# Performance work log

Hardware: AMD Instinct MI355X
Metric: run time of the kernel (lower is better)

Reference implementation:

```python
import jax, jax.numpy as jnp
import numpy as np

H, C = 4, 64          # heads, head_dim; H*C == hidden_channels == 256
HID = H * C
NT, NC = 50000, 10000
E_TT, E_CT = 400000, 200000
FT, FC = 128, 64


def _gat(xs, xd, att_s, att_d, bias, src, dst, num_dst):
    """PyG GATConv message passing. xs/xd: projected feats [Ns,H,C]/[Nd,H,C]."""
    a = (xs * att_s).sum(-1)[src] + (xd * att_d).sum(-1)[dst]      # [E,H]
    a = jax.nn.leaky_relu(a, 0.2)
    m = jax.ops.segment_max(a, dst, num_segments=num_dst)          # [Nd,H]
    m = jnp.where(jnp.isfinite(m), m, 0.0)
    ex = jnp.exp(a - m[dst])                                       # [E,H]
    den = jax.ops.segment_sum(ex, dst, num_segments=num_dst)       # [Nd,H]
    msg = jax.ops.segment_sum(ex[:, :, None] * xs[src], dst, num_segments=num_dst)  # [Nd,H,C]
    out = msg / jnp.maximum(den, 1e-16)[:, :, None]
    return out.reshape(num_dst, HID) + bias


def setup_inputs() -> dict:
    key = jax.random.key(0)
    ks = jax.random.split(key, 24)

    def glorot(k, shape):
        fan_in = shape[0] if len(shape) > 1 else shape[-1]
        return jax.random.normal(k, shape, jnp.float32) / np.sqrt(fan_in)

    inp = {
        'x_target': jax.random.normal(ks[0], (NT, FT), jnp.float32),
        'x_context': jax.random.normal(ks[1], (NC, FC), jnp.float32),
        'ei_tt': jax.random.randint(ks[2], (2, E_TT), 0, NT, jnp.int32),
        'ei_ct_src': jax.random.randint(ks[3], (E_CT,), 0, NC, jnp.int32),
        'ei_ct_dst': jax.random.randint(ks[4], (E_CT,), 0, NT, jnp.int32),
        # HeteroDictLinear pretransform
        'Wt': glorot(ks[5], (FT, HID)), 'bt': jnp.zeros((HID,), jnp.float32),
        'Wc': glorot(ks[6], (FC, HID)), 'bc': jnp.zeros((HID,), jnp.float32),
        # DirGATConv: src->dst GATConv
        'W_s2d': glorot(ks[7], (HID, HID)),
        'as_s2d': glorot(ks[8], (H, C)), 'ad_s2d': glorot(ks[9], (H, C)),
        'b_s2d': jnp.zeros((HID,), jnp.float32),
        # DirGATConv: dst->src GATConv
        'W_d2s': glorot(ks[10], (HID, HID)),
        'as_d2s': glorot(ks[11], (H, C)), 'ad_d2s': glorot(ks[12], (H, C)),
        'b_d2s': jnp.zeros((HID,), jnp.float32),
        # bipartite context->target GATConv
        'W_ct_src': glorot(ks[13], (HID, HID)), 'W_ct_dst': glorot(ks[14], (HID, HID)),
        'as_ct': glorot(ks[15], (H, C)), 'ad_ct': glorot(ks[16], (H, C)),
        'b_ct': jnp.zeros((HID,), jnp.float32),
        # final Linear(hidden, hidden)
        'W_out': glorot(ks[17], (HID, HID)), 'b_out': jnp.zeros((HID,), jnp.float32),
    }
    return inp


def reference(x_target, x_context, ei_tt, ei_ct_src, ei_ct_dst,
              Wt, bt, Wc, bc,
              W_s2d, as_s2d, ad_s2d, b_s2d,
              W_d2s, as_d2s, ad_d2s, b_d2s,
              W_ct_src, W_ct_dst, as_ct, ad_ct, b_ct,
              W_out, b_out):
    nt = x_target.shape[0]
    # HeteroDictLinear pretransform + relu
    ht = jax.nn.relu(x_target @ Wt + bt)      # [NT, HID]
    hc = jax.nn.relu(x_context @ Wc + bc)     # [NC, HID]

    # homogeneous target-target edges with self-loops (PyG GATConv default)
    loops = jnp.arange(nt, dtype=ei_tt.dtype)
    src = jnp.concatenate([ei_tt[0], loops])
    dst = jnp.concatenate([ei_tt[1], loops])

    # DirGATConv: (1-alpha)*conv(x, ei) + alpha*conv(x, ei^T), alpha=0.5
    p1 = (ht @ W_s2d).reshape(nt, H, C)
    out_s2d = _gat(p1, p1, as_s2d, ad_s2d, b_s2d, src, dst, nt)
    p2 = (ht @ W_d2s).reshape(nt, H, C)
    out_d2s = _gat(p2, p2, as_d2s, ad_d2s, b_d2s, dst, src, nt)
    out_tt = 0.5 * out_s2d + 0.5 * out_d2s

    # bipartite context->target GATConv (no self-loops)
    ps = (hc @ W_ct_src).reshape(hc.shape[0], H, C)
    pd = (ht @ W_ct_dst).reshape(nt, H, C)
    out_ct = _gat(ps, pd, as_ct, ad_ct, b_ct, ei_ct_src, ei_ct_dst, nt)

    # HeteroConv aggr='mean', then skip connection + relu, then final Linear
    x = (out_tt + out_ct) * 0.5
    x = jax.nn.relu(x + ht)
    return x @ W_out + b_out
```

## Files before the change

kernel.cpp:

```cpp
#include <hip/hip_runtime.h>
#include <hip/hip_bf16.h>
#include <cstdint>
#include <cstddef>


#define LRELU_SLOPE 0.2f
#define CAP 64
#define NRANGE 8

typedef __attribute__((ext_vector_type(8))) short short8;
typedef __attribute__((ext_vector_type(4))) float floatx4;

__device__ __forceinline__ float bf2f(ushort u) {
    union { unsigned int u32; float f; } v; v.u32 = ((unsigned int)u) << 16; return v.f;
}
__device__ __forceinline__ ushort f2bf(float x) {
    union { float f; unsigned int u; } v; v.f = x;
    unsigned int r = (v.u + 0x7FFFu + ((v.u >> 16) & 1u)) >> 16;
    return (ushort)r;
}

__global__ __launch_bounds__(256) void cast_bf16(
    const float* __restrict__ x, ushort* __restrict__ y, int n4)
{
    const int idx = blockIdx.x * blockDim.x + threadIdx.x;
    if (idx >= n4) return;
    float4 v = ((const float4*)x)[idx];
    ushort4 o;
    o.x = f2bf(v.x); o.y = f2bf(v.y); o.z = f2bf(v.z); o.w = f2bf(v.w);
    ((ushort4*)y)[idx] = o;
}

__global__ __launch_bounds__(256) void wtrans(
    const float* __restrict__ W, ushort* __restrict__ WT, int K)
{
    const int idx = blockIdx.x * blockDim.x + threadIdx.x;
    if (idx >= K * 256) return;
    const int k = idx >> 8, n = idx & 255;
    WT[n * K + k] = f2bf(W[idx]);
}

__global__ __launch_bounds__(256) void gemm_bf16(
    const ushort* __restrict__ A, const ushort* __restrict__ Bt,
    const float* __restrict__ bias, float* __restrict__ Cf,
    ushort* __restrict__ Cb, int M, int K, int do_relu,
    const float* __restrict__ attS, const float* __restrict__ attD,
    float* __restrict__ aSo, float* __restrict__ aDo)
{
    __shared__ short As[64][40];
    __shared__ short Bs[64][40];
    const int tid  = threadIdx.x;
    const int row0 = blockIdx.x * 64;
    const int col0 = blockIdx.y * 64;
    const int lr = tid >> 2;
    const int lk = (tid & 3) * 8;
    const int w    = tid >> 6;
    const int lane = tid & 63;
    const int mrow = 16 * w + (lane & 15);
    const int ksel = (lane >> 4) * 8;

    floatx4 acc0 = {0.f,0.f,0.f,0.f}, acc1 = acc0, acc2 = acc0, acc3 = acc0;

    for (int k0 = 0; k0 < K; k0 += 32) {
        short8 av = {0,0,0,0,0,0,0,0};
        if (row0 + lr < M)
            av = *(const short8*)(A + (size_t)(row0 + lr) * K + k0 + lk);
        *(short8*)&As[lr][lk] = av;
        *(short8*)&Bs[lr][lk] =
            *(const short8*)(Bt + (size_t)(col0 + lr) * K + k0 + lk);
        __syncthreads();
        short8 af = *(const short8*)&As[mrow][ksel];
        short8 b0 = *(const short8*)&Bs[ 0 + (lane & 15)][ksel];
        short8 b1 = *(const short8*)&Bs[16 + (lane & 15)][ksel];
        short8 b2 = *(const short8*)&Bs[32 + (lane & 15)][ksel];
        short8 b3 = *(const short8*)&Bs[48 + (lane & 15)][ksel];
        acc0 = __builtin_amdgcn_mfma_f32_16x16x32_bf16(af, b0, acc0, 0, 0, 0);
        acc1 = __builtin_amdgcn_mfma_f32_16x16x32_bf16(af, b1, acc1, 0, 0, 0);
        acc2 = __builtin_amdgcn_mfma_f32_16x16x32_bf16(af, b2, acc2, 0, 0, 0);
        acc3 = __builtin_amdgcn_mfma_f32_16x16x32_bf16(af, b3, acc3, 0, 0, 0);
        __syncthreads();
    }

    const int rbase = row0 + 16 * w + (lane >> 4) * 4;
    floatx4 av[4] = {acc0, acc1, acc2, acc3};
#pragma unroll
    for (int c = 0; c < 4; ++c) {
        const int col = col0 + 16 * c + (lane & 15);
        const float bv = bias ? bias[col] : 0.f;
#pragma unroll
        for (int i = 0; i < 4; ++i) {
            const int row = rbase + i;
            if (row < M) {
                float v = av[c][i] + bv;
                if (do_relu) v = fmaxf(v, 0.f);
                const size_t off = (size_t)row * 256 + col;
                if (Cf) Cf[off] = v;
                if (Cb) Cb[off] = f2bf(v);
            }
        }
    }

    if (attS) {
        const int cix = lane & 15;
        float sA[4] = {0.f,0.f,0.f,0.f}, sD[4] = {0.f,0.f,0.f,0.f};
#pragma unroll
        for (int c = 0; c < 4; ++c) {
            const float as_v = attS[col0 + 16 * c + cix];
            const float ad_v = attD ? attD[col0 + 16 * c + cix] : 0.f;
#pragma unroll
            for (int i = 0; i < 4; ++i) {
                sA[i] += av[c][i] * as_v;
                sD[i] += av[c][i] * ad_v;
            }
        }
#pragma unroll
        for (int off = 1; off < 16; off <<= 1) {
#pragma unroll
            for (int i = 0; i < 4; ++i) {
                sA[i] += __shfl_xor(sA[i], off);
                sD[i] += __shfl_xor(sD[i], off);
            }
        }
        if (cix == 0) {
            const int head = col0 >> 6;
#pragma unroll
            for (int i = 0; i < 4; ++i) {
                const int row = rbase + i;
                if (row < M) {
                    aSo[(size_t)row * 4 + head] = sA[i];
                    if (aDo) aDo[(size_t)row * 4 + head] = sD[i];
                }
            }
        }
    }
}

__global__ void fold_ct(const float* __restrict__ W, const float* __restrict__ ad,
                        float* __restrict__ wfold)
{
    int idx = blockIdx.x * blockDim.x + threadIdx.x;
    if (idx >= 1024) return;
    int k = idx >> 2, h = idx & 3;
    float s = 0.f;
#pragma unroll 8
    for (int c = 0; c < 64; ++c) s += W[(size_t)k * 256 + h * 64 + c] * ad[h * 64 + c];
    wfold[idx] = s;
}

__global__ __launch_bounds__(256) void alpha_from_fold(
    const ushort* __restrict__ ht, const float* __restrict__ wfold,
    float* __restrict__ aD, int N)
{
    __shared__ float wf[1024];
    const int tid = threadIdx.x;
    *(float4*)&wf[tid * 4] = *(const float4*)&wfold[tid * 4];
    __syncthreads();
    const int idx = blockIdx.x * 256 + tid;
    if (idx >= N * 4) return;
    const int n = idx >> 2, h = idx & 3;
    const ushort* row = ht + (size_t)n * 256;
    float s = 0.f;
#pragma unroll
    for (int k = 0; k < 256; k += 4) {
        ushort4 r4 = *(const ushort4*)(row + k);
        s += bf2f(r4.x) * wf[(k + 0) * 4 + h] + bf2f(r4.y) * wf[(k + 1) * 4 + h]
           + bf2f(r4.z) * wf[(k + 2) * 4 + h] + bf2f(r4.w) * wf[(k + 3) * 4 + h];
    }
    aD[idx] = s;
}

__global__ __launch_bounds__(256) void build_buckets_tt_ranged(
    const int* __restrict__ src, const int* __restrict__ dst, int E, int RS,
    int* __restrict__ cntA, int* __restrict__ bktA,
    int* __restrict__ cntB, int* __restrict__ bktB)
{
    const int range = blockIdx.x & (NRANGE - 1);
    const int lo = range * RS, hi = lo + RS;
    const int nb = gridDim.x >> 3;
    const int j  = blockIdx.x >> 3;
    const int stride = nb * blockDim.x;
    for (int e = j * blockDim.x + threadIdx.x; e < E; e += stride) {
        const int s = src[e], d = dst[e];
        if (d >= lo && d < hi) {
            const int pa = atomicAdd(&cntA[d], 1);
            if (pa < CAP) bktA[(size_t)d * CAP + pa] = s;
        }
        if (s >= lo && s < hi) {
            const int pb = atomicAdd(&cntB[s], 1);
            if (pb < CAP) bktB[(size_t)s * CAP + pb] = d;
        }
    }
}

__global__ __launch_bounds__(256) void build_bucket_ranged(
    const int* __restrict__ src, const int* __restrict__ dst, int E, int RS,
    int* __restrict__ cnt, int* __restrict__ bkt)
{
    const int range = blockIdx.x & (NRANGE - 1);
    const int lo = range * RS, hi = lo + RS;
    const int nb = gridDim.x >> 3;
    const int j  = blockIdx.x >> 3;
    const int stride = nb * blockDim.x;
    for (int e = j * blockDim.x + threadIdx.x; e < E; e += stride) {
        const int s = src[e], d = dst[e];
        if (d >= lo && d < hi) {
            const int p = atomicAdd(&cnt[d], 1);
            if (p < CAP) bkt[(size_t)d * CAP + p] = s;
        }
    }
}

__device__ __forceinline__ void gat_phase(
    int n, int h, int c4,
    const int* __restrict__ cnt, const int* __restrict__ bkt,
    const float* __restrict__ aS, const float* __restrict__ aD,
    const ushort* __restrict__ X, const float* __restrict__ bias,
    float scale, int has_self, float4& out)
{
    const float aDn = aD[(size_t)n * 4 + h];
    float4 f = {0.f, 0.f, 0.f, 0.f};
    float den = 0.f;
    if (has_self) {
        float a = aS[(size_t)n * 4 + h] + aDn;
        a = (a >= 0.f) ? a : LRELU_SLOPE * a;
        const float w = __expf(a);
        const ushort4 x = *(const ushort4*)(X + (size_t)n * 256 + c4);
        f.x = w * bf2f(x.x); f.y = w * bf2f(x.y);
        f.z = w * bf2f(x.z); f.w = w * bf2f(x.w);
        den = w;
    }
    const int deg = min(cnt[n], CAP);
    const int* b = bkt + (size_t)n * CAP;
    int i = 0;
    for (; i + 4 <= deg; i += 4) {
        const int s0 = b[i], s1 = b[i + 1], s2 = b[i + 2], s3 = b[i + 3];
        float a0 = aS[(size_t)s0 * 4 + h] + aDn;
        float a1 = aS[(size_t)s1 * 4 + h] + aDn;
        float a2 = aS[(size_t)s2 * 4 + h] + aDn;
        float a3 = aS[(size_t)s3 * 4 + h] + aDn;
        a0 = (a0 >= 0.f) ? a0 : LRELU_SLOPE * a0;
        a1 = (a1 >= 0.f) ? a1 : LRELU_SLOPE * a1;
        a2 = (a2 >= 0.f) ? a2 : LRELU_SLOPE * a2;
        a3 = (a3 >= 0.f) ? a3 : LRELU_SLOPE * a3;
        const float w0 = __expf(a0), w1 = __expf(a1);
        const float w2 = __expf(a2), w3 = __expf(a3);
        const ushort4 x0 = *(const ushort4*)(X + (size_t)s0 * 256 + c4);
        const ushort4 x1 = *(const ushort4*)(X + (size_t)s1 * 256 + c4);
        const ushort4 x2 = *(const ushort4*)(X + (size_t)s2 * 256 + c4);
        const ushort4 x3 = *(const ushort4*)(X + (size_t)s3 * 256 + c4);
        f.x += w0 * bf2f(x0.x) + w1 * bf2f(x1.x) + w2 * bf2f(x2.x) + w3 * bf2f(x3.x);
        f.y += w0 * bf2f(x0.y) + w1 * bf2f(x1.y) + w2 * bf2f(x2.y) + w3 * bf2f(x3.y);
        f.z += w0 * bf2f(x0.z) + w1 * bf2f(x1.z) + w2 * bf2f(x2.z) + w3 * bf2f(x3.z);
        f.w += w0 * bf2f(x0.w) + w1 * bf2f(x1.w) + w2 * bf2f(x2.w) + w3 * bf2f(x3.w);
        den += w0 + w1 + w2 + w3;
    }
    for (; i < deg; ++i) {
        const int s = b[i];
        float a = aS[(size_t)s * 4 + h] + aDn;
        a = (a >= 0.f) ? a : LRELU_SLOPE * a;
        const float w = __expf(a);
        const ushort4 x = *(const ushort4*)(X + (size_t)s * 256 + c4);
        f.x += w * bf2f(x.x); f.y += w * bf2f(x.y);
        f.z += w * bf2f(x.z); f.w += w * bf2f(x.w);
        den += w;
    }
    const float inv = 1.f / fmaxf(den, 1e-16f);
    const float4 bv = *(const float4*)(bias + c4);
    out.x += scale * (f.x * inv + bv.x);
    out.y += scale * (f.y * inv + bv.y);
    out.z += scale * (f.z * inv + bv.z);
    out.w += scale * (f.w * inv + bv.w);
}

__global__ __launch_bounds__(256) void gat_gather_fused(
    const int* __restrict__ cntA, const int* __restrict__ bktA,
    const float* __restrict__ aS1, const float* __restrict__ aD1,
    const ushort* __restrict__ P1, const float* __restrict__ b1,
    const int* __restrict__ cntB, const int* __restrict__ bktB,
    const float* __restrict__ aS2, const float* __restrict__ aD2,
    const ushort* __restrict__ P2, const float* __restrict__ b2,
    const int* __restrict__ cntC, const int* __restrict__ bktC,
    const float* __restrict__ aSc, const float* __restrict__ aDc,
    const ushort* __restrict__ Pc, const float* __restrict__ b3,
    ushort* __restrict__ htb, int N)
{
    const int n = blockIdx.x * 4 + (threadIdx.x >> 6);
    if (n >= N) return;
    const int lane = threadIdx.x & 63;
    const int h  = lane >> 4;
    const int c4 = lane << 2;

    float4 out = {0.f, 0.f, 0.f, 0.f};
    gat_phase(n, h, c4, cntA, bktA, aS1, aD1, P1, b1, 0.25f, 1, out);
    gat_phase(n, h, c4, cntB, bktB, aS2, aD2, P2, b2, 0.25f, 1, out);
    gat_phase(n, h, c4, cntC, bktC, aSc, aDc, Pc, b3, 0.50f, 0, out);

    ushort* hp = htb + (size_t)n * 256 + c4;
    const ushort4 hb = *(const ushort4*)hp;
    ushort4 o;
    o.x = f2bf(fmaxf(out.x + bf2f(hb.x), 0.f));
    o.y = f2bf(fmaxf(out.y + bf2f(hb.y), 0.f));
    o.z = f2bf(fmaxf(out.z + bf2f(hb.z), 0.f));
    o.w = f2bf(fmaxf(out.w + bf2f(hb.w), 0.f));
    *(ushort4*)hp = o;
}

extern "C" void kernel_launch(void* const* d_in, const int* in_sizes, int n_in,
                              void* d_out, int out_size, void* d_ws, size_t ws_size,
                              hipStream_t stream)
{
    const int NT   = in_sizes[0] / 128;
    const int NC   = in_sizes[1] / 64;
    const int E_TT = in_sizes[2] / 2;
    const int E_CT = in_sizes[3];

    const float* x_target = (const float*)d_in[0];
    const float* x_context= (const float*)d_in[1];
    const int*   ei_tt    = (const int*)d_in[2];
    const int*   ei_ct_src= (const int*)d_in[3];
    const int*   ei_ct_dst= (const int*)d_in[4];
    const float* Wt   = (const float*)d_in[5];
    const float* bt   = (const float*)d_in[6];
    const float* Wc   = (const float*)d_in[7];
    const float* bc   = (const float*)d_in[8];
    const float* W_s2d  = (const float*)d_in[9];
    const float* as_s2d = (const float*)d_in[10];
    const float* ad_s2d = (const float*)d_in[11];
    const float* b_s2d  = (const float*)d_in[12];
    const float* W_d2s  = (const float*)d_in[13];
    const float* as_d2s = (const float*)d_in[14];
    const float* ad_d2s = (const float*)d_in[15];
    const float* b_d2s  = (const float*)d_in[16];
    const float* W_ct_src = (const float*)d_in[17];
    const float* W_ct_dst = (const float*)d_in[18];
    const float* as_ct  = (const float*)d_in[19];
    const float* ad_ct  = (const float*)d_in[20];
    const float* b_ct   = (const float*)d_in[21];
    const float* W_out  = (const float*)d_in[22];
    const float* b_out  = (const float*)d_in[23];
    float* out = (float*)d_out;

    const int* tt_src = ei_tt;
    const int* tt_dst = ei_tt + E_TT;

    float* ws = (float*)d_ws;
    size_t o = 0;
    ushort* htb = (ushort*)(ws + o);   o += (size_t)NT * 128;
    ushort* Pb1 = (ushort*)(ws + o);   o += (size_t)NT * 128;
    ushort* Pb2 = (ushort*)(ws + o);   o += (size_t)NT * 128;
    ushort* hcb = (ushort*)(ws + o);   o += (size_t)NC * 128;
    ushort* PSb = (ushort*)(ws + o);   o += (size_t)NC * 128;
    ushort* xtb = (ushort*)(ws + o);   o += (size_t)NT * 64;
    ushort* xcb = (ushort*)(ws + o);   o += (size_t)NC * 32;
    int* bktA = (int*)(ws + o);        o += (size_t)NT * CAP;
    int* bktB = (int*)(ws + o);        o += (size_t)NT * CAP;
    int* bktC = (int*)(ws + o);        o += (size_t)NT * CAP;
    float* aS1 = ws + o;               o += (size_t)NT * 4;
    float* aD1 = ws + o;               o += (size_t)NT * 4;
    float* aS2 = ws + o;               o += (size_t)NT * 4;
    float* aD2 = ws + o;               o += (size_t)NT * 4;
    float* aSc = ws + o;               o += (size_t)NT * 4;
    float* aDc = ws + o;               o += (size_t)NT * 4;
    int*   cntA = (int*)(ws + o);      o += (size_t)NT;
    int*   cntB = (int*)(ws + o);      o += (size_t)NT;
    int*   cntC = (int*)(ws + o);      o += (size_t)NT;
    float* wfold = ws + o;             o += 1024;
    ushort* WtT   = (ushort*)(ws + o); o += 128 * 256 / 2;
    ushort* WcT   = (ushort*)(ws + o); o += 64 * 256 / 2;
    ushort* Ws2dT = (ushort*)(ws + o); o += 256 * 256 / 2;
    ushort* Wd2sT = (ushort*)(ws + o); o += 256 * 256 / 2;
    ushort* WctsT = (ushort*)(ws + o); o += 256 * 256 / 2;
    ushort* WoutT = (ushort*)(ws + o); o += 256 * 256 / 2;
    (void)ws_size; (void)n_in; (void)out_size;

    const dim3 blk(256);
    const int gN4 = (NT * 4 + 255) / 256;
    const int gGat = (NT + 3) / 4;
    const int RS = (NT + NRANGE - 1) / NRANGE;

    auto gemm = [&](const ushort* A, const ushort* Bt, const float* bias,
                    float* Cf, ushort* Cb, int M, int K, int relu,
                    const float* attS, const float* attD, float* aSo, float* aDo) {
        dim3 grid((M + 63) / 64, 4);
        hipLaunchKernelGGL(gemm_bf16, grid, blk, 0, stream, A, Bt, bias, Cf, Cb,
                           M, K, relu, attS, attD, aSo, aDo);
    };

    hipMemsetAsync(cntA, 0, (size_t)NT * 3 * sizeof(int), stream);
    hipLaunchKernelGGL(cast_bf16, dim3((NT * 128 / 4 + 255) / 256), blk, 0, stream,
                       x_target, xtb, NT * 128 / 4);
    hipLaunchKernelGGL(cast_bf16, dim3((NC * 64 / 4 + 255) / 256), blk, 0, stream,
                       x_context, xcb, NC * 64 / 4);
    hipLaunchKernelGGL(wtrans, dim3(128), blk, 0, stream, Wt, WtT, 128);
    hipLaunchKernelGGL(wtrans, dim3(64),  blk, 0, stream, Wc, WcT, 64);
    hipLaunchKernelGGL(wtrans, dim3(256), blk, 0, stream, W_s2d, Ws2dT, 256);
    hipLaunchKernelGGL(wtrans, dim3(256), blk, 0, stream, W_d2s, Wd2sT, 256);
    hipLaunchKernelGGL(wtrans, dim3(256), blk, 0, stream, W_ct_src, WctsT, 256);
    hipLaunchKernelGGL(wtrans, dim3(256), blk, 0, stream, W_out, WoutT, 256);
    hipLaunchKernelGGL(build_buckets_tt_ranged, dim3(64 * NRANGE), blk, 0, stream,
                       tt_src, tt_dst, E_TT, RS, cntA, bktA, cntB, bktB);
    hipLaunchKernelGGL(build_bucket_ranged, dim3(64 * NRANGE), blk, 0, stream,
                       ei_ct_src, ei_ct_dst, E_CT, RS, cntC, bktC);

    gemm(xtb, WtT, bt, nullptr, htb, NT, 128, 1, nullptr, nullptr, nullptr, nullptr);
    gemm(xcb, WcT, bc, nullptr, hcb, NC, 64, 1, nullptr, nullptr, nullptr, nullptr);

    gemm(htb, Ws2dT, nullptr, nullptr, Pb1, NT, 256, 0, as_s2d, ad_s2d, aS1, aD1);
    gemm(htb, Wd2sT, nullptr, nullptr, Pb2, NT, 256, 0, as_d2s, ad_d2s, aS2, aD2);
    gemm(hcb, WctsT, nullptr, nullptr, PSb, NC, 256, 0, as_ct, nullptr, aSc, nullptr);
    hipLaunchKernelGGL(fold_ct, dim3(4), blk, 0, stream, W_ct_dst, ad_ct, wfold);
    hipLaunchKernelGGL(alpha_from_fold, dim3(gN4), blk, 0, stream, htb, wfold, aDc, NT);

    hipLaunchKernelGGL(gat_gather_fused, dim3(gGat), blk, 0, stream,
                       cntA, bktA, aS1, aD1, Pb1, b_s2d,
                       cntB, bktB, aS2, aD2, Pb2, b_d2s,
                       cntC, bktC, aSc, aDc, PSb, b_ct,
                       htb, NT);

    gemm(htb, WoutT, b_out, out, nullptr, NT, 256, 0, nullptr, nullptr, nullptr, nullptr);
}
```

Before: 451.2 us.

## Compute full 256-column GEMM rows per block and batch GAT gathers by eight

The GEMM now covers all 256 output columns in one block (16 MFMA accumulators per wave), so the A tile is loaded once instead of four times and the attention dot products for all heads come from a single block. The GAT aggregation hoists the per-node degree and attention scalars and adds an 8-wide unrolled gather loop to keep more loads in flight. The trade is higher register pressure (64 accumulator floats plus the attention partials), a 4x smaller grid that may underfill the GPU for smaller M, and larger shared memory use.

```diff
diff --git a/kernel.cpp b/kernel.cpp
--- a/kernel.cpp
+++ b/kernel.cpp
@@ -48,50 +48,50 @@
     float* __restrict__ aSo, float* __restrict__ aDo)
 {
     __shared__ short As[64][40];
-    __shared__ short Bs[64][40];
+    __shared__ short Bs[256][40];
     const int tid  = threadIdx.x;
     const int row0 = blockIdx.x * 64;
-    const int col0 = blockIdx.y * 64;
     const int lr = tid >> 2;
     const int lk = (tid & 3) * 8;
     const int w    = tid >> 6;
     const int lane = tid & 63;
-    const int mrow = 16 * w + (lane & 15);
+    const int cix  = lane & 15;
+    const int mrow = 16 * w + cix;
     const int ksel = (lane >> 4) * 8;
 
-    floatx4 acc0 = {0.f,0.f,0.f,0.f}, acc1 = acc0, acc2 = acc0, acc3 = acc0;
+    floatx4 acc[16];
+#pragma unroll
+    for (int c = 0; c < 16; ++c) acc[c] = (floatx4){0.f, 0.f, 0.f, 0.f};
 
     for (int k0 = 0; k0 < K; k0 += 32) {
         short8 av = {0,0,0,0,0,0,0,0};
         if (row0 + lr < M)
             av = *(const short8*)(A + (size_t)(row0 + lr) * K + k0 + lk);
         *(short8*)&As[lr][lk] = av;
-        *(short8*)&Bs[lr][lk] =
-            *(const short8*)(Bt + (size_t)(col0 + lr) * K + k0 + lk);
+#pragma unroll
+        for (int q = 0; q < 4; ++q)
+            *(short8*)&Bs[lr + 64 * q][lk] =
+                *(const short8*)(Bt + (size_t)(lr + 64 * q) * K + k0 + lk);
         __syncthreads();
-        short8 af = *(const short8*)&As[mrow][ksel];
-        short8 b0 = *(const short8*)&Bs[ 0 + (lane & 15)][ksel];
-        short8 b1 = *(const short8*)&Bs[16 + (lane & 15)][ksel];
-        short8 b2 = *(const short8*)&Bs[32 + (lane & 15)][ksel];
-        short8 b3 = *(const short8*)&Bs[48 + (lane & 15)][ksel];
-        acc0 = __builtin_amdgcn_mfma_f32_16x16x32_bf16(af, b0, acc0, 0, 0, 0);
-        acc1 = __builtin_amdgcn_mfma_f32_16x16x32_bf16(af, b1, acc1, 0, 0, 0);
-        acc2 = __builtin_amdgcn_mfma_f32_16x16x32_bf16(af, b2, acc2, 0, 0, 0);
-        acc3 = __builtin_amdgcn_mfma_f32_16x16x32_bf16(af, b3, acc3, 0, 0, 0);
+        const short8 af = *(const short8*)&As[mrow][ksel];
+#pragma unroll
+        for (int c = 0; c < 16; ++c) {
+            const short8 bf = *(const short8*)&Bs[16 * c + cix][ksel];
+            acc[c] = __builtin_amdgcn_mfma_f32_16x16x32_bf16(af, bf, acc[c], 0, 0, 0);
+        }
         __syncthreads();
     }
 
     const int rbase = row0 + 16 * w + (lane >> 4) * 4;
-    floatx4 av[4] = {acc0, acc1, acc2, acc3};
-#pragma unroll
-    for (int c = 0; c < 4; ++c) {
-        const int col = col0 + 16 * c + (lane & 15);
+#pragma unroll
+    for (int c = 0; c < 16; ++c) {
+        const int col = 16 * c + cix;
         const float bv = bias ? bias[col] : 0.f;
 #pragma unroll
         for (int i = 0; i < 4; ++i) {
             const int row = rbase + i;
             if (row < M) {
-                float v = av[c][i] + bv;
+                float v = acc[c][i] + bv;
                 if (do_relu) v = fmaxf(v, 0.f);
                 const size_t off = (size_t)row * 256 + col;
                 if (Cf) Cf[off] = v;
@@ -101,34 +101,42 @@
     }
 
     if (attS) {
-        const int cix = lane & 15;
-        float sA[4] = {0.f,0.f,0.f,0.f}, sD[4] = {0.f,0.f,0.f,0.f};
-#pragma unroll
-        for (int c = 0; c < 4; ++c) {
-            const float as_v = attS[col0 + 16 * c + cix];
-            const float ad_v = attD ? attD[col0 + 16 * c + cix] : 0.f;
+        float sA[4][4], sD[4][4];
+#pragma unroll
+        for (int h = 0; h < 4; ++h)
+#pragma unroll
+            for (int i = 0; i < 4; ++i) { sA[h][i] = 0.f; sD[h][i] = 0.f; }
+#pragma unroll
+        for (int c = 0; c < 16; ++c) {
+            const int h = c >> 2;
+            const float as_v = attS[16 * c + cix];
+            const float ad_v = attD ? attD[16 * c + cix] : 0.f;
 #pragma unroll
             for (int i = 0; i < 4; ++i) {
-                sA[i] += av[c][i] * as_v;
-                sD[i] += av[c][i] * ad_v;
+                sA[h][i] += acc[c][i] * as_v;
+                sD[h][i] += acc[c][i] * ad_v;
             }
         }
 #pragma unroll
         for (int off = 1; off < 16; off <<= 1) {
 #pragma unroll
-            for (int i = 0; i < 4; ++i) {
-                sA[i] += __shfl_xor(sA[i], off);
-                sD[i] += __shfl_xor(sD[i], off);
-            }
+            for (int h = 0; h < 4; ++h)
+#pragma unroll
+                for (int i = 0; i < 4; ++i) {
+                    sA[h][i] += __shfl_xor(sA[h][i], off);
+                    sD[h][i] += __shfl_xor(sD[h][i], off);
+                }
         }
         if (cix == 0) {
-            const int head = col0 >> 6;
 #pragma unroll
             for (int i = 0; i < 4; ++i) {
                 const int row = rbase + i;
                 if (row < M) {
-                    aSo[(size_t)row * 4 + head] = sA[i];
-                    if (aDo) aDo[(size_t)row * 4 + head] = sD[i];
+#pragma unroll
+                    for (int h = 0; h < 4; ++h) {
+                        aSo[(size_t)row * 4 + h] = sA[h][i];
+                        if (aDo) aDo[(size_t)row * 4 + h] = sD[h][i];
+                    }
                 }
             }
         }
@@ -211,17 +219,16 @@
 }
 
 __device__ __forceinline__ void gat_phase(
-    int n, int h, int c4,
-    const int* __restrict__ cnt, const int* __restrict__ bkt,
-    const float* __restrict__ aS, const float* __restrict__ aD,
+    int n, int h, int c4, int deg,
+    const int* __restrict__ bkt,
+    const float* __restrict__ aS, float aSn_self, float aDn,
     const ushort* __restrict__ X, const float* __restrict__ bias,
     float scale, int has_self, float4& out)
 {
-    const float aDn = aD[(size_t)n * 4 + h];
     float4 f = {0.f, 0.f, 0.f, 0.f};
     float den = 0.f;
     if (has_self) {
-        float a = aS[(size_t)n * 4 + h] + aDn;
+        float a = aSn_self + aDn;
         a = (a >= 0.f) ? a : LRELU_SLOPE * a;
         const float w = __expf(a);
         const ushort4 x = *(const ushort4*)(X + (size_t)n * 256 + c4);
@@ -229,30 +236,55 @@
         f.z = w * bf2f(x.z); f.w = w * bf2f(x.w);
         den = w;
     }
-    const int deg = min(cnt[n], CAP);
     const int* b = bkt + (size_t)n * CAP;
     int i = 0;
+    for (; i + 8 <= deg; i += 8) {
+        int s[8];
+#pragma unroll
+        for (int j = 0; j < 8; ++j) s[j] = b[i + j];
+        float wv[8];
+#pragma unroll
+        for (int j = 0; j < 8; ++j) {
+            float a = aS[(size_t)s[j] * 4 + h] + aDn;
+            a = (a >= 0.f) ? a : LRELU_SLOPE * a;
+            wv[j] = __expf(a);
+        }
+        ushort4 x[8];
+#pragma unroll
+        for (int j = 0; j < 8; ++j)
+            x[j] = *(const ushort4*)(X + (size_t)s[j] * 256 + c4);
+#pragma unroll
+        for (int j = 0; j < 8; ++j) {
+            f.x += wv[j] * bf2f(x[j].x);
+            f.y += wv[j] * bf2f(x[j].y);
+            f.z += wv[j] * bf2f(x[j].z);
+            f.w += wv[j] * bf2f(x[j].w);
+            den += wv[j];
+        }
+    }
     for (; i + 4 <= deg; i += 4) {
-        const int s0 = b[i], s1 = b[i + 1], s2 = b[i + 2], s3 = b[i + 3];
-        float a0 = aS[(size_t)s0 * 4 + h] + aDn;
-        float a1 = aS[(size_t)s1 * 4 + h] + aDn;
-        float a2 = aS[(size_t)s2 * 4 + h] + aDn;
-        float a3 = aS[(size_t)s3 * 4 + h] + aDn;
-        a0 = (a0 >= 0.f) ? a0 : LRELU_SLOPE * a0;
-        a1 = (a1 >= 0.f) ? a1 : LRELU_SLOPE * a1;
-        a2 = (a2 >= 0.f) ? a2 : LRELU_SLOPE * a2;
-        a3 = (a3 >= 0.f) ? a3 : LRELU_SLOPE * a3;
-        const float w0 = __expf(a0), w1 = __expf(a1);
-        const float w2 = __expf(a2), w3 = __expf(a3);
-        const ushort4 x0 = *(const ushort4*)(X + (size_t)s0 * 256 + c4);
-        const ushort4 x1 = *(const ushort4*)(X + (size_t)s1 * 256 + c4);
-        const ushort4 x2 = *(const ushort4*)(X + (size_t)s2 * 256 + c4);
-        const ushort4 x3 = *(const ushort4*)(X + (size_t)s3 * 256 + c4);
-        f.x += w0 * bf2f(x0.x) + w1 * bf2f(x1.x) + w2 * bf2f(x2.x) + w3 * bf2f(x3.x);
-        f.y += w0 * bf2f(x0.y) + w1 * bf2f(x1.y) + w2 * bf2f(x2.y) + w3 * bf2f(x3.y);
-        f.z += w0 * bf2f(x0.z) + w1 * bf2f(x1.z) + w2 * bf2f(x2.z) + w3 * bf2f(x3.z);
-        f.w += w0 * bf2f(x0.w) + w1 * bf2f(x1.w) + w2 * bf2f(x2.w) + w3 * bf2f(x3.w);
-        den += w0 + w1 + w2 + w3;
+        int s[4];
+#pragma unroll
+        for (int j = 0; j < 4; ++j) s[j] = b[i + j];
+        float wv[4];
+#pragma unroll
+        for (int j = 0; j < 4; ++j) {
+            float a = aS[(size_t)s[j] * 4 + h] + aDn;
+            a = (a >= 0.f) ? a : LRELU_SLOPE * a;
+            wv[j] = __expf(a);
+        }
+        ushort4 x[4];
+#pragma unroll
+        for (int j = 0; j < 4; ++j)
+            x[j] = *(const ushort4*)(X + (size_t)s[j] * 256 + c4);
+#pragma unroll
+        for (int j = 0; j < 4; ++j) {
+            f.x += wv[j] * bf2f(x[j].x);
+            f.y += wv[j] * bf2f(x[j].y);
+            f.z += wv[j] * bf2f(x[j].z);
+            f.w += wv[j] * bf2f(x[j].w);
+            den += wv[j];
+        }
     }
     for (; i < deg; ++i) {
         const int s = b[i];
@@ -290,10 +322,19 @@
     const int h  = lane >> 4;
     const int c4 = lane << 2;
 
+    const int degA = min(cntA[n], CAP);
+    const int degB = min(cntB[n], CAP);
+    const int degC = min(cntC[n], CAP);
+    const float aD1n = aD1[(size_t)n * 4 + h];
+    const float aD2n = aD2[(size_t)n * 4 + h];
+    const float aDcn = aDc[(size_t)n * 4 + h];
+    const float aS1n = aS1[(size_t)n * 4 + h];
+    const float aS2n = aS2[(size_t)n * 4 + h];
+
     float4 out = {0.f, 0.f, 0.f, 0.f};
-    gat_phase(n, h, c4, cntA, bktA, aS1, aD1, P1, b1, 0.25f, 1, out);
-    gat_phase(n, h, c4, cntB, bktB, aS2, aD2, P2, b2, 0.25f, 1, out);
-    gat_phase(n, h, c4, cntC, bktC, aSc, aDc, Pc, b3, 0.50f, 0, out);
+    gat_phase(n, h, c4, degA, bktA, aS1, aS1n, aD1n, P1, b1, 0.25f, 1, out);
+    gat_phase(n, h, c4, degB, bktB, aS2, aS2n, aD2n, P2, b2, 0.25f, 1, out);
+    gat_phase(n, h, c4, degC, bktC, aSc, 0.f, aDcn, Pc, b3, 0.50f, 0, out);
 
     ushort* hp = htb + (size_t)n * 256 + c4;
     const ushort4 hb = *(const ushort4*)hp;
@@ -381,7 +422,7 @@
     auto gemm = [&](const ushort* A, const ushort* Bt, const float* bias,
                     float* Cf, ushort* Cb, int M, int K, int relu,
                     const float* attS, const float* attD, float* aSo, float* aDo) {
-        dim3 grid((M + 63) / 64, 4);
+        dim3 grid((M + 63) / 64);
         hipLaunchKernelGGL(gemm_bf16, grid, blk, 0, stream, A, Bt, bias, Cf, Cb,
                            M, K, relu, attS, attD, aSo, aDo);
     };
```

Result: slower. 564.6 us (+25.1%).
